# Performance work log

Hardware: AMD Instinct MI355X
Metric: run time of the kernel (lower is better)

Reference implementation:

```python
import jax, jax.numpy as jnp
import numpy as np

B, T, C, H = 4, 2048, 1024, 128

def setup_inputs() -> dict:
    key = jax.random.key(0)
    k1, k2, k3, k4 = jax.random.split(key, 4)
    x = jax.random.normal(k1, (B, T, C), dtype=jnp.float32)
    # nn.Linear(C, H, bias=False) weights, stored as [C, H] so y = x @ W
    scale = 1.0 / np.sqrt(C)
    Wq = jax.random.normal(k2, (C, H), dtype=jnp.float32) * scale
    Wk = jax.random.normal(k3, (C, H), dtype=jnp.float32) * scale
    Wv = jax.random.normal(k4, (C, H), dtype=jnp.float32) * scale
    mask = jnp.tril(jnp.ones((T, T), dtype=jnp.int32))  # causal mask
    return {"x": x, "Wq": Wq, "Wk": Wk, "Wv": Wv, "mask": mask}

def reference(x, Wq, Wk, Wv, mask):
    # x: [B,T,C]; projections to [B,T,H]
    q = jnp.einsum("btc,ch->bth", x, Wq)
    k = jnp.einsum("btc,ch->bth", x, Wk)
    v = jnp.einsum("btc,ch->bth", x, Wv)
    # NOTE: original scales by C**-0.5 (embedding dim), not head_size**-0.5
    inv_scale = x.shape[-1] ** (-0.5)
    scores = jnp.einsum("bth,bsh->bts", q, k) * inv_scale  # [B,T,T]
    scores = jnp.where(mask == 0, -jnp.inf, scores)
    weights = jax.nn.softmax(scores, axis=-1)
    # Dropout(0.1) is identity in eval mode
    return jnp.einsum("bts,bsh->bth", weights, v)  # [B,T,H]
```

## Files before the change

kernel.cpp:

```cpp
#include <hip/hip_runtime.h>
#include <hip/hip_bf16.h>
#include <cstdint>


typedef __bf16 bf16_t;
typedef __bf16 bf16x4 __attribute__((ext_vector_type(4)));
typedef __bf16 bf16x8 __attribute__((ext_vector_type(8)));
typedef float f32x4 __attribute__((ext_vector_type(4)));

#define MFMA16(a, b, c) __builtin_amdgcn_mfma_f32_16x16x32_bf16(a, b, c, 0, 0, 0)

constexpr int T = 2048;
constexpr int C = 1024;
constexpr int H = 128;
constexpr int BK = 64;

__device__ inline bf16x8 load8f(const float* __restrict__ p) {
    float4 a = *(const float4*)p;
    float4 b = *(const float4*)(p + 4);
    bf16x8 r;
    r[0] = (bf16_t)a.x; r[1] = (bf16_t)a.y; r[2] = (bf16_t)a.z; r[3] = (bf16_t)a.w;
    r[4] = (bf16_t)b.x; r[5] = (bf16_t)b.y; r[6] = (bf16_t)b.z; r[7] = (bf16_t)b.w;
    return r;
}

__device__ inline void gld16(const bf16_t* g, bf16_t* l) {
    __builtin_amdgcn_global_load_lds(
        (const __attribute__((address_space(1))) unsigned int*)g,
        (__attribute__((address_space(3))) unsigned int*)l, 16, 0, 0);
}

__global__ __launch_bounds__(256) void prep(const float* __restrict__ x,
                                            const float* __restrict__ Wq,
                                            const float* __restrict__ Wk,
                                            const float* __restrict__ Wv,
                                            bf16_t* __restrict__ xb,
                                            bf16_t* __restrict__ Wt) {
    const int t = threadIdx.x;
    if (blockIdx.x < 2048) {
        const int n8 = 4 * T * C / 8;
        int i = blockIdx.x * 256 + t;
        for (; i < n8; i += 2048 * 256)
            *(bf16x8*)(xb + (size_t)i * 8) = load8f(x + (size_t)i * 8);
    } else {
        __shared__ bf16_t tile[32][34];
        const int b2 = blockIdx.x - 2048;
        const int z = b2 >> 7, rem = b2 & 127;
        const int c0 = (rem & 31) * 32, h0 = (rem >> 5) * 32;
        const float* W = z == 0 ? Wq : (z == 1 ? Wk : Wv);
        const int tx = t & 31, ty = t >> 5;
#pragma unroll
        for (int i = 0; i < 4; i++)
            tile[ty + 8 * i][tx] = (bf16_t)W[(size_t)(c0 + ty + 8 * i) * H + h0 + tx];
        __syncthreads();
        bf16_t* Wtz = Wt + (size_t)z * H * C;
#pragma unroll
        for (int i = 0; i < 4; i++)
            Wtz[(size_t)(h0 + ty + 8 * i) * C + c0 + tx] = tile[tx][ty + 8 * i];
    }
}

__global__ __launch_bounds__(256) void proj_gemm(const bf16_t* __restrict__ xb,
                                                 const bf16_t* __restrict__ Wt,
                                                 bf16_t* __restrict__ qout,
                                                 bf16_t* __restrict__ kout,
                                                 bf16_t* __restrict__ vtout) {
    __shared__ __align__(16) bf16_t Ab[2][64 * BK];
    __shared__ __align__(16) bf16_t Bb[2][128 * BK];
    const int t = threadIdx.x;
    const int w = t >> 6, lane = t & 63;
    const int m16 = lane & 15, g = lane >> 4;
    const int wm = w & 1, wn = w >> 1;
    const int z = blockIdx.y;
    const int m0 = blockIdx.x * 64;
    const bf16_t* Bsrc = Wt + (size_t)z * H * C;

    auto stage = [&](int s, int k0) {
#pragma unroll
        for (int i = 0; i < 2; i++) {
            const int e = i * 256 + t;
            const int r = e >> 3, v = e & 7, c8 = v ^ (r & 7);
            gld16(xb + (size_t)(m0 + r) * C + k0 + c8 * 8,
                  &Ab[s][(i * 4 + w) * 512]);
        }
#pragma unroll
        for (int i = 0; i < 4; i++) {
            const int e = i * 256 + t;
            const int r = e >> 3, v = e & 7, c8 = v ^ (r & 7);
            gld16(Bsrc + (size_t)r * C + k0 + c8 * 8,
                  &Bb[s][(i * 4 + w) * 512]);
        }
    };

    f32x4 zero = {0.f, 0.f, 0.f, 0.f};
    f32x4 acc[2][4];
#pragma unroll
    for (int mf = 0; mf < 2; mf++)
#pragma unroll
        for (int nf = 0; nf < 4; nf++) acc[mf][nf] = zero;

    stage(0, 0);
    for (int c = 0; c < C / BK; c++) {
        __syncthreads();
        if (c + 1 < C / BK) stage((c + 1) & 1, (c + 1) * BK);
        const int s = c & 1;

        bf16x8 af[2][2], bfr[4][2];
#pragma unroll
        for (int mf = 0; mf < 2; mf++)
#pragma unroll
            for (int kf = 0; kf < 2; kf++) {
                const int r = wm * 32 + mf * 16 + m16;
                const int v = (kf * 4 + g) ^ (r & 7);
                af[mf][kf] = *(const bf16x8*)(&Ab[s][r * BK + v * 8]);
            }
#pragma unroll
        for (int nf = 0; nf < 4; nf++)
#pragma unroll
            for (int kf = 0; kf < 2; kf++) {
                const int r = wn * 64 + nf * 16 + m16;
                const int v = (kf * 4 + g) ^ (r & 7);
                bfr[nf][kf] = *(const bf16x8*)(&Bb[s][r * BK + v * 8]);
            }
#pragma unroll
        for (int kf = 0; kf < 2; kf++)
#pragma unroll
            for (int mf = 0; mf < 2; mf++)
#pragma unroll
                for (int nf = 0; nf < 4; nf++)
                    acc[mf][nf] = MFMA16(af[mf][kf], bfr[nf][kf], acc[mf][nf]);
    }

    const float sc = (z == 0) ? 0.03125f : 1.0f;
    if (z < 2) {
        bf16_t* out = (z == 0) ? qout : kout;
#pragma unroll
        for (int mf = 0; mf < 2; mf++)
#pragma unroll
            for (int nf = 0; nf < 4; nf++)
#pragma unroll
                for (int ri = 0; ri < 4; ri++) {
                    const int r = m0 + wm * 32 + mf * 16 + g * 4 + ri;
                    const int n = wn * 64 + nf * 16 + m16;
                    out[(size_t)r * H + n] = (bf16_t)(acc[mf][nf][ri] * sc);
                }
    } else {
#pragma unroll
        for (int mf = 0; mf < 2; mf++) {
            const int t0 = m0 + wm * 32 + mf * 16 + g * 4;
            const int bidx = t0 >> 11, tt = t0 & (T - 1);
#pragma unroll
            for (int nf = 0; nf < 4; nf++) {
                const int h = wn * 64 + nf * 16 + m16;
                bf16x4 vv;
#pragma unroll
                for (int ri = 0; ri < 4; ri++) vv[ri] = (bf16_t)acc[mf][nf][ri];
                *(bf16x4*)(vtout + ((size_t)bidx * H + h) * T + tt) = vv;
            }
        }
    }
}

__global__ __launch_bounds__(256) void attn(const bf16_t* __restrict__ q,
                                            const bf16_t* __restrict__ k,
                                            const bf16_t* __restrict__ vt,
                                            float* __restrict__ out) {
    __shared__ float accw[4][16][128];
    __shared__ __align__(16) bf16_t pbuf[4][16][40];
    __shared__ float mred[4][16], lred[4][16];
    const int w = threadIdx.x >> 6;
    const int lane = threadIdx.x & 63;
    const int m16 = lane & 15, g = lane >> 4;
    const int b = blockIdx.x & 3;
    const int kk = blockIdx.x >> 2;
    const int qt = (kk < 64) ? kk : 191 - kk;
    const int q0 = qt * 16;

    const bf16_t* qb = q + (size_t)b * T * H;
    const bf16_t* kb = k + (size_t)b * T * H;
    const bf16_t* vb = vt + (size_t)b * H * T;

    bf16x8 aq[4];
#pragma unroll
    for (int c = 0; c < 4; c++)
        aq[c] = *(const bf16x8*)(qb + (size_t)(q0 + m16) * H + c * 32 + g * 8);

    bf16x8 ones;
#pragma unroll
    for (int j = 0; j < 8; j++) ones[j] = (bf16_t)1.0f;

    f32x4 zero = {0.f, 0.f, 0.f, 0.f};
    f32x4 acc[9];
#pragma unroll
    for (int ht = 0; ht < 9; ht++) acc[ht] = zero;
    float mst[4];
#pragma unroll
    for (int ri = 0; ri < 4; ri++) mst[ri] = -1e30f;

    const int kv_end = q0 + 16;
    bf16x8 kc[8], kn[8], vc[8];
    int kv0 = w * 32;
    if (kv0 < kv_end) {
#pragma unroll
        for (int t = 0; t < 2; t++)
#pragma unroll
            for (int c = 0; c < 4; c++)
                kc[t * 4 + c] = *(const bf16x8*)(kb + (size_t)(kv0 + t * 16 + m16) * H + c * 32 + g * 8);
    }

    for (; kv0 < kv_end; kv0 += 128) {
        f32x4 s[2];
        s[0] = zero; s[1] = zero;
#pragma unroll
        for (int t = 0; t < 2; t++)
#pragma unroll
            for (int c = 0; c < 4; c++)
                s[t] = MFMA16(aq[c], kc[t * 4 + c], s[t]);

#pragma unroll
        for (int ht = 0; ht < 8; ht++)
            vc[ht] = *(const bf16x8*)(vb + (size_t)(ht * 16 + m16) * T + kv0 + g * 8);

        const int kvn = kv0 + 128;
        if (kvn < kv_end) {
#pragma unroll
            for (int t = 0; t < 2; t++)
#pragma unroll
                for (int c = 0; c < 4; c++)
                    kn[t * 4 + c] = *(const bf16x8*)(kb + (size_t)(kvn + t * 16 + m16) * H + c * 32 + g * 8);
        }

        float p0v[4], p1v[4];
#pragma unroll
        for (int ri = 0; ri < 4; ri++) {
            const int row = q0 + g * 4 + ri;
            float v0 = s[0][ri];
            float v1 = s[1][ri];
            if (kv0 + m16 > row) v0 = -1e30f;
            if (kv0 + 16 + m16 > row) v1 = -1e30f;
            float rm = fmaxf(v0, v1);
#pragma unroll
            for (int off = 1; off < 16; off <<= 1) rm = fmaxf(rm, __shfl_xor(rm, off));
            const float mnew = fmaxf(mst[ri], rm);
            const float alpha = __expf(mst[ri] - mnew);
            mst[ri] = mnew;
            p0v[ri] = __expf(v0 - mnew);
            p1v[ri] = __expf(v1 - mnew);
#pragma unroll
            for (int ht = 0; ht < 9; ht++) acc[ht][ri] *= alpha;
        }

#pragma unroll
        for (int ri = 0; ri < 4; ri++) {
            pbuf[w][g * 4 + ri][m16] = (bf16_t)p0v[ri];
            pbuf[w][g * 4 + ri][16 + m16] = (bf16_t)p1v[ri];
        }
        bf16x8 ap = *(const bf16x8*)(&pbuf[w][m16][g * 8]);

#pragma unroll
        for (int ht = 0; ht < 8; ht++)
            acc[ht] = MFMA16(ap, vc[ht], acc[ht]);
        acc[8] = MFMA16(ap, ones, acc[8]);

#pragma unroll
        for (int i = 0; i < 8; i++) kc[i] = kn[i];
    }

    if (m16 == 0) {
#pragma unroll
        for (int ri = 0; ri < 4; ri++) mred[w][g * 4 + ri] = mst[ri];
    }
    __syncthreads();
    float scale[4];
#pragma unroll
    for (int ri = 0; ri < 4; ri++) {
        const int row = g * 4 + ri;
        float mt = fmaxf(fmaxf(mred[0][row], mred[1][row]),
                         fmaxf(mred[2][row], mred[3][row]));
        scale[ri] = __expf(mst[ri] - mt);
    }
    if (m16 == 0) {
#pragma unroll
        for (int ri = 0; ri < 4; ri++) lred[w][g * 4 + ri] = acc[8][ri] * scale[ri];
    }
#pragma unroll
    for (int ht = 0; ht < 8; ht++)
#pragma unroll
        for (int ri = 0; ri < 4; ri++)
            accw[w][g * 4 + ri][ht * 16 + m16] = acc[ht][ri] * scale[ri];
    __syncthreads();

    float* ob = out + ((size_t)b * T + q0) * H;
    for (int e = threadIdx.x; e < 16 * 128; e += 256) {
        const int row = e >> 7, col = e & 127;
        float o = accw[0][row][col] + accw[1][row][col] +
                  accw[2][row][col] + accw[3][row][col];
        float l = lred[0][row] + lred[1][row] + lred[2][row] + lred[3][row];
        ob[(size_t)row * H + col] = o / l;
    }
}

extern "C" void kernel_launch(void* const* d_in, const int* in_sizes, int n_in,
                              void* d_out, int out_size, void* d_ws, size_t ws_size,
                              hipStream_t stream) {
    const float* x = (const float*)d_in[0];
    const float* Wq = (const float*)d_in[1];
    const float* Wk = (const float*)d_in[2];
    const float* Wv = (const float*)d_in[3];
    float* out = (float*)d_out;

    char* ws = (char*)d_ws;
    bf16_t* xb = (bf16_t*)ws;
    bf16_t* Wt = (bf16_t*)(ws + 16777216);
    char* p = ws + 16777216 + 786432;
    bf16_t* qb = (bf16_t*)(p);
    bf16_t* kb = (bf16_t*)(p + 2097152);
    bf16_t* vt = (bf16_t*)(p + 2 * 2097152);

    hipLaunchKernelGGL(prep, dim3(2048 + 384), dim3(256), 0, stream,
                       x, Wq, Wk, Wv, xb, Wt);
    hipLaunchKernelGGL(proj_gemm, dim3(128, 3), dim3(256), 0, stream,
                       xb, Wt, qb, kb, vt);
    hipLaunchKernelGGL(attn, dim3(512), dim3(256), 0, stream,
                       qb, kb, vt, out);
}
```

Baseline: 140.7 us.

## Process 32 query rows per attention block to reuse K/V loads

Measured after the change: 146.7 us. 1.04x slower.

```diff
diff --git a/kernel.cpp b/kernel.cpp
--- a/kernel.cpp
+++ b/kernel.cpp
@@ -80,15 +80,13 @@
         for (int i = 0; i < 2; i++) {
             const int e = i * 256 + t;
             const int r = e >> 3, v = e & 7, c8 = v ^ (r & 7);
-            gld16(xb + (size_t)(m0 + r) * C + k0 + c8 * 8,
-                  &Ab[s][(i * 4 + w) * 512]);
+            gld16(xb + (size_t)(m0 + r) * C + k0 + c8 * 8, &Ab[s][(i * 4 + w) * 512]);
         }
 #pragma unroll
         for (int i = 0; i < 4; i++) {
             const int e = i * 256 + t;
             const int r = e >> 3, v = e & 7, c8 = v ^ (r & 7);
-            gld16(Bsrc + (size_t)r * C + k0 + c8 * 8,
-                  &Bb[s][(i * 4 + w) * 512]);
+            gld16(Bsrc + (size_t)r * C + k0 + c8 * 8, &Bb[s][(i * 4 + w) * 512]);
         }
     };
 
@@ -161,43 +159,48 @@
     }
 }
 
-__global__ __launch_bounds__(256) void attn(const bf16_t* __restrict__ q,
-                                            const bf16_t* __restrict__ k,
-                                            const bf16_t* __restrict__ vt,
-                                            float* __restrict__ out) {
-    __shared__ float accw[4][16][128];
-    __shared__ __align__(16) bf16_t pbuf[4][16][40];
-    __shared__ float mred[4][16], lred[4][16];
+__global__ __launch_bounds__(256, 1) void attn(const bf16_t* __restrict__ q,
+                                               const bf16_t* __restrict__ k,
+                                               const bf16_t* __restrict__ vt,
+                                               float* __restrict__ out) {
+    __shared__ float accw[4][32][128];
+    __shared__ __align__(16) bf16_t pbuf[4][32][40];
+    __shared__ float mred[4][32], lred[4][32];
     const int w = threadIdx.x >> 6;
     const int lane = threadIdx.x & 63;
     const int m16 = lane & 15, g = lane >> 4;
     const int b = blockIdx.x & 3;
-    const int kk = blockIdx.x >> 2;
-    const int qt = (kk < 64) ? kk : 191 - kk;
-    const int q0 = qt * 16;
+    const int j = blockIdx.x >> 2;
+    const int q0 = j * 32;
 
     const bf16_t* qb = q + (size_t)b * T * H;
     const bf16_t* kb = k + (size_t)b * T * H;
     const bf16_t* vb = vt + (size_t)b * H * T;
 
-    bf16x8 aq[4];
-#pragma unroll
-    for (int c = 0; c < 4; c++)
-        aq[c] = *(const bf16x8*)(qb + (size_t)(q0 + m16) * H + c * 32 + g * 8);
+    bf16x8 aq[2][4];
+#pragma unroll
+    for (int mf = 0; mf < 2; mf++)
+#pragma unroll
+        for (int c = 0; c < 4; c++)
+            aq[mf][c] = *(const bf16x8*)(qb + (size_t)(q0 + mf * 16 + m16) * H + c * 32 + g * 8);
 
     bf16x8 ones;
 #pragma unroll
-    for (int j = 0; j < 8; j++) ones[j] = (bf16_t)1.0f;
+    for (int i = 0; i < 8; i++) ones[i] = (bf16_t)1.0f;
 
     f32x4 zero = {0.f, 0.f, 0.f, 0.f};
-    f32x4 acc[9];
-#pragma unroll
-    for (int ht = 0; ht < 9; ht++) acc[ht] = zero;
-    float mst[4];
-#pragma unroll
-    for (int ri = 0; ri < 4; ri++) mst[ri] = -1e30f;
-
-    const int kv_end = q0 + 16;
+    f32x4 acc[2][9];
+#pragma unroll
+    for (int mf = 0; mf < 2; mf++)
+#pragma unroll
+        for (int ht = 0; ht < 9; ht++) acc[mf][ht] = zero;
+    float mst[2][4];
+#pragma unroll
+    for (int mf = 0; mf < 2; mf++)
+#pragma unroll
+        for (int ri = 0; ri < 4; ri++) mst[mf][ri] = -1e30f;
+
+    const int kv_end = q0 + 32;
     bf16x8 kc[8], kn[8], vc[8];
     int kv0 = w * 32;
     if (kv0 < kv_end) {
@@ -209,18 +212,21 @@
     }
 
     for (; kv0 < kv_end; kv0 += 128) {
-        f32x4 s[2];
-        s[0] = zero; s[1] = zero;
+        f32x4 s[2][2];
+#pragma unroll
+        for (int mf = 0; mf < 2; mf++) { s[mf][0] = zero; s[mf][1] = zero; }
 #pragma unroll
         for (int t = 0; t < 2; t++)
 #pragma unroll
-            for (int c = 0; c < 4; c++)
-                s[t] = MFMA16(aq[c], kc[t * 4 + c], s[t]);
+            for (int c = 0; c < 4; c++) {
+#pragma unroll
+                for (int mf = 0; mf < 2; mf++)
+                    s[mf][t] = MFMA16(aq[mf][c], kc[t * 4 + c], s[mf][t]);
+            }
 
 #pragma unroll
         for (int ht = 0; ht < 8; ht++)
             vc[ht] = *(const bf16x8*)(vb + (size_t)(ht * 16 + m16) * T + kv0 + g * 8);
-
         const int kvn = kv0 + 128;
         if (kvn < kv_end) {
 #pragma unroll
@@ -230,68 +236,80 @@
                     kn[t * 4 + c] = *(const bf16x8*)(kb + (size_t)(kvn + t * 16 + m16) * H + c * 32 + g * 8);
         }
 
-        float p0v[4], p1v[4];
+#pragma unroll
+        for (int mf = 0; mf < 2; mf++) {
+            float p0v[4], p1v[4];
+#pragma unroll
+            for (int ri = 0; ri < 4; ri++) {
+                const int row = q0 + mf * 16 + g * 4 + ri;
+                float v0 = s[mf][0][ri];
+                float v1 = s[mf][1][ri];
+                if (kv0 + m16 > row) v0 = -1e30f;
+                if (kv0 + 16 + m16 > row) v1 = -1e30f;
+                float rm = fmaxf(v0, v1);
+#pragma unroll
+                for (int off = 1; off < 16; off <<= 1) rm = fmaxf(rm, __shfl_xor(rm, off));
+                const float mnew = fmaxf(mst[mf][ri], rm);
+                const float alpha = __expf(mst[mf][ri] - mnew);
+                mst[mf][ri] = mnew;
+                p0v[ri] = __expf(v0 - mnew);
+                p1v[ri] = __expf(v1 - mnew);
+#pragma unroll
+                for (int ht = 0; ht < 9; ht++) acc[mf][ht][ri] *= alpha;
+            }
+#pragma unroll
+            for (int ri = 0; ri < 4; ri++) {
+                pbuf[w][mf * 16 + g * 4 + ri][m16] = (bf16_t)p0v[ri];
+                pbuf[w][mf * 16 + g * 4 + ri][16 + m16] = (bf16_t)p1v[ri];
+            }
+        }
+
+#pragma unroll
+        for (int mf = 0; mf < 2; mf++) {
+            bf16x8 ap = *(const bf16x8*)(&pbuf[w][mf * 16 + m16][g * 8]);
+#pragma unroll
+            for (int ht = 0; ht < 8; ht++)
+                acc[mf][ht] = MFMA16(ap, vc[ht], acc[mf][ht]);
+            acc[mf][8] = MFMA16(ap, ones, acc[mf][8]);
+        }
+
+#pragma unroll
+        for (int i = 0; i < 8; i++) kc[i] = kn[i];
+    }
+
+    if (m16 == 0) {
+#pragma unroll
+        for (int mf = 0; mf < 2; mf++)
+#pragma unroll
+            for (int ri = 0; ri < 4; ri++)
+                mred[w][mf * 16 + g * 4 + ri] = mst[mf][ri];
+    }
+    __syncthreads();
+#pragma unroll
+    for (int mf = 0; mf < 2; mf++) {
+        float scale[4];
 #pragma unroll
         for (int ri = 0; ri < 4; ri++) {
-            const int row = q0 + g * 4 + ri;
-            float v0 = s[0][ri];
-            float v1 = s[1][ri];
-            if (kv0 + m16 > row) v0 = -1e30f;
-            if (kv0 + 16 + m16 > row) v1 = -1e30f;
-            float rm = fmaxf(v0, v1);
-#pragma unroll
-            for (int off = 1; off < 16; off <<= 1) rm = fmaxf(rm, __shfl_xor(rm, off));
-            const float mnew = fmaxf(mst[ri], rm);
-            const float alpha = __expf(mst[ri] - mnew);
-            mst[ri] = mnew;
-            p0v[ri] = __expf(v0 - mnew);
-            p1v[ri] = __expf(v1 - mnew);
-#pragma unroll
-            for (int ht = 0; ht < 9; ht++) acc[ht][ri] *= alpha;
-        }
-
-#pragma unroll
-        for (int ri = 0; ri < 4; ri++) {
-            pbuf[w][g * 4 + ri][m16] = (bf16_t)p0v[ri];
-            pbuf[w][g * 4 + ri][16 + m16] = (bf16_t)p1v[ri];
-        }
-        bf16x8 ap = *(const bf16x8*)(&pbuf[w][m16][g * 8]);
-
+            const int row = mf * 16 + g * 4 + ri;
+            float mt = fmaxf(fmaxf(mred[0][row], mred[1][row]),
+                             fmaxf(mred[2][row], mred[3][row]));
+            scale[ri] = __expf(mst[mf][ri] - mt);
+        }
+        if (m16 == 0) {
+#pragma unroll
+            for (int ri = 0; ri < 4; ri++)
+                lred[w][mf * 16 + g * 4 + ri] = acc[mf][8][ri] * scale[ri];
+        }
 #pragma unroll
         for (int ht = 0; ht < 8; ht++)
-            acc[ht] = MFMA16(ap, vc[ht], acc[ht]);
-        acc[8] = MFMA16(ap, ones, acc[8]);
-
-#pragma unroll
-        for (int i = 0; i < 8; i++) kc[i] = kn[i];
-    }
-
-    if (m16 == 0) {
-#pragma unroll
-        for (int ri = 0; ri < 4; ri++) mred[w][g * 4 + ri] = mst[ri];
+#pragma unroll
+            for (int ri = 0; ri < 4; ri++)
+                accw[w][mf * 16 + g * 4 + ri][ht * 16 + m16] = acc[mf][ht][ri] * scale[ri];
     }
     __syncthreads();
-    float scale[4];
-#pragma unroll
-    for (int ri = 0; ri < 4; ri++) {
-        const int row = g * 4 + ri;
-        float mt = fmaxf(fmaxf(mred[0][row], mred[1][row]),
-                         fmaxf(mred[2][row], mred[3][row]));
-        scale[ri] = __expf(mst[ri] - mt);
-    }
-    if (m16 == 0) {
-#pragma unroll
-        for (int ri = 0; ri < 4; ri++) lred[w][g * 4 + ri] = acc[8][ri] * scale[ri];
-    }
-#pragma unroll
-    for (int ht = 0; ht < 8; ht++)
-#pragma unroll
-        for (int ri = 0; ri < 4; ri++)
-            accw[w][g * 4 + ri][ht * 16 + m16] = acc[ht][ri] * scale[ri];
-    __syncthreads();
 
     float* ob = out + ((size_t)b * T + q0) * H;
-    for (int e = threadIdx.x; e < 16 * 128; e += 256) {
+    for (int e = threadIdx.x; e < 32 * 128; e += 256) {
         const int row = e >> 7, col = e & 127;
         float o = accw[0][row][col] + accw[1][row][col] +
                   accw[2][row][col] + accw[3][row][col];
@@ -321,6 +339,6 @@
                        x, Wq, Wk, Wv, xb, Wt);
     hipLaunchKernelGGL(proj_gemm, dim3(128, 3), dim3(256), 0, stream,
                        xb, Wt, qb, kb, vt);
-    hipLaunchKernelGGL(attn, dim3(512), dim3(256), 0, stream,
+    hipLaunchKernelGGL(attn, dim3(256), dim3(256), 0, stream,
                        qb, kb, vt, out);
 }
```

## Fuse prep, projection GEMM and attention into one persistent kernel with grid barriers

Applied to the files above, without the earlier changes.

New measurement: 322.6 us. 129% more time.

```diff
diff --git a/kernel.cpp b/kernel.cpp
--- a/kernel.cpp
+++ b/kernel.cpp
@@ -15,288 +15,299 @@
 constexpr int H = 128;
 constexpr int BK = 64;
 
-__device__ inline bf16x8 load8f(const float* __restrict__ p) {
-    float4 a = *(const float4*)p;
-    float4 b = *(const float4*)(p + 4);
-    bf16x8 r;
-    r[0] = (bf16_t)a.x; r[1] = (bf16_t)a.y; r[2] = (bf16_t)a.z; r[3] = (bf16_t)a.w;
-    r[4] = (bf16_t)b.x; r[5] = (bf16_t)b.y; r[6] = (bf16_t)b.z; r[7] = (bf16_t)b.w;
-    return r;
-}
-
-__device__ inline void gld16(const bf16_t* g, bf16_t* l) {
+__device__ inline void gld16(const void* g, void* l) {
     __builtin_amdgcn_global_load_lds(
         (const __attribute__((address_space(1))) unsigned int*)g,
         (__attribute__((address_space(3))) unsigned int*)l, 16, 0, 0);
 }
 
-__global__ __launch_bounds__(256) void prep(const float* __restrict__ x,
-                                            const float* __restrict__ Wq,
-                                            const float* __restrict__ Wk,
-                                            const float* __restrict__ Wv,
-                                            bf16_t* __restrict__ xb,
-                                            bf16_t* __restrict__ Wt) {
-    const int t = threadIdx.x;
-    if (blockIdx.x < 2048) {
-        const int n8 = 4 * T * C / 8;
-        int i = blockIdx.x * 256 + t;
-        for (; i < n8; i += 2048 * 256)
-            *(bf16x8*)(xb + (size_t)i * 8) = load8f(x + (size_t)i * 8);
-    } else {
-        __shared__ bf16_t tile[32][34];
-        const int b2 = blockIdx.x - 2048;
-        const int z = b2 >> 7, rem = b2 & 127;
+__device__ inline void gbar(int* cnt, int target) {
+    __syncthreads();
+    if (threadIdx.x == 0) {
+        __threadfence();
+        __hip_atomic_fetch_add(cnt, 1, __ATOMIC_ACQ_REL, __HIP_MEMORY_SCOPE_AGENT);
+        while (__hip_atomic_load(cnt, __ATOMIC_ACQUIRE, __HIP_MEMORY_SCOPE_AGENT) < target)
+            __builtin_amdgcn_s_sleep(8);
+        __threadfence();
+    }
+    __syncthreads();
+}
+
+union SMem {
+    struct { bf16_t tile[32][34]; } tr;
+    struct { float Ab[2][64 * BK]; bf16_t Bb[2][128 * BK]; } pj;
+    struct {
+        float accw[4][16][128];
+        bf16_t pbuf[4][16][40];
+        float mred[4][16], lred[4][16];
+    } at;
+};
+
+__global__ __launch_bounds__(256, 2) void fused(const float* __restrict__ x,
+                                                const float* __restrict__ Wq,
+                                                const float* __restrict__ Wk,
+                                                const float* __restrict__ Wv,
+                                                bf16_t* __restrict__ Wt,
+                                                bf16_t* __restrict__ qb_,
+                                                bf16_t* __restrict__ kb_,
+                                                bf16_t* __restrict__ vt_,
+                                                float* __restrict__ out,
+                                                int* __restrict__ flag) {
+    __shared__ __align__(16) SMem sm;
+    const int tid = threadIdx.x;
+    const int blk = blockIdx.x;
+
+    if (blk < 384) {
+        const int z = blk >> 7, rem = blk & 127;
         const int c0 = (rem & 31) * 32, h0 = (rem >> 5) * 32;
         const float* W = z == 0 ? Wq : (z == 1 ? Wk : Wv);
-        const int tx = t & 31, ty = t >> 5;
+        const int tx = tid & 31, ty = tid >> 5;
 #pragma unroll
         for (int i = 0; i < 4; i++)
-            tile[ty + 8 * i][tx] = (bf16_t)W[(size_t)(c0 + ty + 8 * i) * H + h0 + tx];
+            sm.tr.tile[ty + 8 * i][tx] = (bf16_t)W[(size_t)(c0 + ty + 8 * i) * H + h0 + tx];
         __syncthreads();
         bf16_t* Wtz = Wt + (size_t)z * H * C;
 #pragma unroll
         for (int i = 0; i < 4; i++)
-            Wtz[(size_t)(h0 + ty + 8 * i) * C + c0 + tx] = tile[tx][ty + 8 * i];
+            Wtz[(size_t)(h0 + ty + 8 * i) * C + c0 + tx] = sm.tr.tile[tx][ty + 8 * i];
     }
-}
-
-__global__ __launch_bounds__(256) void proj_gemm(const bf16_t* __restrict__ xb,
-                                                 const bf16_t* __restrict__ Wt,
-                                                 bf16_t* __restrict__ qout,
-                                                 bf16_t* __restrict__ kout,
-                                                 bf16_t* __restrict__ vtout) {
-    __shared__ __align__(16) bf16_t Ab[2][64 * BK];
-    __shared__ __align__(16) bf16_t Bb[2][128 * BK];
-    const int t = threadIdx.x;
-    const int w = t >> 6, lane = t & 63;
-    const int m16 = lane & 15, g = lane >> 4;
-    const int wm = w & 1, wn = w >> 1;
-    const int z = blockIdx.y;
-    const int m0 = blockIdx.x * 64;
-    const bf16_t* Bsrc = Wt + (size_t)z * H * C;
-
-    auto stage = [&](int s, int k0) {
-#pragma unroll
-        for (int i = 0; i < 2; i++) {
-            const int e = i * 256 + t;
-            const int r = e >> 3, v = e & 7, c8 = v ^ (r & 7);
-            gld16(xb + (size_t)(m0 + r) * C + k0 + c8 * 8,
-                  &Ab[s][(i * 4 + w) * 512]);
-        }
-#pragma unroll
-        for (int i = 0; i < 4; i++) {
-            const int e = i * 256 + t;
-            const int r = e >> 3, v = e & 7, c8 = v ^ (r & 7);
-            gld16(Bsrc + (size_t)r * C + k0 + c8 * 8,
-                  &Bb[s][(i * 4 + w) * 512]);
-        }
-    };
-
-    f32x4 zero = {0.f, 0.f, 0.f, 0.f};
-    f32x4 acc[2][4];
-#pragma unroll
-    for (int mf = 0; mf < 2; mf++)
-#pragma unroll
-        for (int nf = 0; nf < 4; nf++) acc[mf][nf] = zero;
-
-    stage(0, 0);
-    for (int c = 0; c < C / BK; c++) {
+    gbar(flag, 512);
+
+    if (blk < 384) {
+        const int w = tid >> 6, lane = tid & 63;
+        const int m16 = lane & 15, g = lane >> 4;
+        const int wm = w & 1, wn = w >> 1;
+        const int z = blk >> 7;
+        const int m0 = (blk & 127) * 64;
+        const bf16_t* Bsrc = Wt + (size_t)z * H * C;
+
+        auto stage = [&](int s, int k0) {
+#pragma unroll
+            for (int i = 0; i < 4; i++) {
+                const int e = i * 256 + tid;
+                const int r = e >> 4, v = e & 15, c4 = v ^ (r & 15);
+                gld16(x + (size_t)(m0 + r) * C + k0 + c4 * 4,
+                      &sm.pj.Ab[s][(i * 4 + w) * 256]);
+            }
+#pragma unroll
+            for (int i = 0; i < 4; i++) {
+                const int e = i * 256 + tid;
+                const int r = e >> 3, v = e & 7, c8 = v ^ (r & 7);
+                gld16(Bsrc + (size_t)r * C + k0 + c8 * 8,
+                      &sm.pj.Bb[s][(i * 4 + w) * 512]);
+            }
+        };
+
+        f32x4 zero = {0.f, 0.f, 0.f, 0.f};
+        f32x4 acc[2][4];
+#pragma unroll
+        for (int mf = 0; mf < 2; mf++)
+#pragma unroll
+            for (int nf = 0; nf < 4; nf++) acc[mf][nf] = zero;
+
+        stage(0, 0);
+        for (int c = 0; c < C / BK; c++) {
+            __syncthreads();
+            if (c + 1 < C / BK) stage((c + 1) & 1, (c + 1) * BK);
+            const int s = c & 1;
+
+            bf16x8 af[2][2], bfr[4][2];
+#pragma unroll
+            for (int mf = 0; mf < 2; mf++)
+#pragma unroll
+                for (int kf = 0; kf < 2; kf++) {
+                    const int r = wm * 32 + mf * 16 + m16;
+                    const int c4 = kf * 8 + g * 2;
+                    const int va = c4 ^ (r & 15), vb = (c4 + 1) ^ (r & 15);
+                    float4 fa = *(const float4*)(&sm.pj.Ab[s][r * BK + va * 4]);
+                    float4 fb = *(const float4*)(&sm.pj.Ab[s][r * BK + vb * 4]);
+                    bf16x8 t;
+                    t[0] = (bf16_t)fa.x; t[1] = (bf16_t)fa.y;
+                    t[2] = (bf16_t)fa.z; t[3] = (bf16_t)fa.w;
+                    t[4] = (bf16_t)fb.x; t[5] = (bf16_t)fb.y;
+                    t[6] = (bf16_t)fb.z; t[7] = (bf16_t)fb.w;
+                    af[mf][kf] = t;
+                }
+#pragma unroll
+            for (int nf = 0; nf < 4; nf++)
+#pragma unroll
+                for (int kf = 0; kf < 2; kf++) {
+                    const int r = wn * 64 + nf * 16 + m16;
+                    const int v = (kf * 4 + g) ^ (r & 7);
+                    bfr[nf][kf] = *(const bf16x8*)(&sm.pj.Bb[s][r * BK + v * 8]);
+                }
+#pragma unroll
+            for (int kf = 0; kf < 2; kf++)
+#pragma unroll
+                for (int mf = 0; mf < 2; mf++)
+#pragma unroll
+                    for (int nf = 0; nf < 4; nf++)
+                        acc[mf][nf] = MFMA16(af[mf][kf], bfr[nf][kf], acc[mf][nf]);
+        }
+
+        const float sc = (z == 0) ? 0.03125f : 1.0f;
+        if (z < 2) {
+            bf16_t* o = (z == 0) ? qb_ : kb_;
+#pragma unroll
+            for (int mf = 0; mf < 2; mf++)
+#pragma unroll
+                for (int nf = 0; nf < 4; nf++)
+#pragma unroll
+                    for (int ri = 0; ri < 4; ri++) {
+                        const int r = m0 + wm * 32 + mf * 16 + g * 4 + ri;
+                        const int n = wn * 64 + nf * 16 + m16;
+                        o[(size_t)r * H + n] = (bf16_t)(acc[mf][nf][ri] * sc);
+                    }
+        } else {
+#pragma unroll
+            for (int mf = 0; mf < 2; mf++) {
+                const int t0 = m0 + wm * 32 + mf * 16 + g * 4;
+                const int bidx = t0 >> 11, tt = t0 & (T - 1);
+#pragma unroll
+                for (int nf = 0; nf < 4; nf++) {
+                    const int h = wn * 64 + nf * 16 + m16;
+                    bf16x4 vv;
+#pragma unroll
+                    for (int ri = 0; ri < 4; ri++) vv[ri] = (bf16_t)acc[mf][nf][ri];
+                    *(bf16x4*)(vt_ + ((size_t)bidx * H + h) * T + tt) = vv;
+                }
+            }
+        }
+    }
+    gbar(flag, 1024);
+
+    {
+        const int w = tid >> 6;
+        const int lane = tid & 63;
+        const int m16 = lane & 15, g = lane >> 4;
+        const int b = blk & 3;
+        const int kk = blk >> 2;
+        const int qt = (kk < 64) ? kk : 191 - kk;
+        const int q0 = qt * 16;
+
+        const bf16_t* qb = qb_ + (size_t)b * T * H;
+        const bf16_t* kb = kb_ + (size_t)b * T * H;
+        const bf16_t* vb = vt_ + (size_t)b * H * T;
+
+        bf16x8 aq[4];
+#pragma unroll
+        for (int c = 0; c < 4; c++)
+            aq[c] = *(const bf16x8*)(qb + (size_t)(q0 + m16) * H + c * 32 + g * 8);
+
+        bf16x8 ones;
+#pragma unroll
+        for (int i = 0; i < 8; i++) ones[i] = (bf16_t)1.0f;
+
+        f32x4 zero = {0.f, 0.f, 0.f, 0.f};
+        f32x4 acc[9];
+#pragma unroll
+        for (int ht = 0; ht < 9; ht++) acc[ht] = zero;
+        float mst[4];
+#pragma unroll
+        for (int ri = 0; ri < 4; ri++) mst[ri] = -1e30f;
+
+        const int kv_end = q0 + 16;
+        bf16x8 kc[8], kn[8], vc[8];
+        int kv0 = w * 32;
+        if (kv0 < kv_end) {
+#pragma unroll
+            for (int t = 0; t < 2; t++)
+#pragma unroll
+                for (int c = 0; c < 4; c++)
+                    kc[t * 4 + c] = *(const bf16x8*)(kb + (size_t)(kv0 + t * 16 + m16) * H + c * 32 + g * 8);
+        }
+
+        for (; kv0 < kv_end; kv0 += 128) {
+            f32x4 s[2];
+            s[0] = zero; s[1] = zero;
+#pragma unroll
+            for (int t = 0; t < 2; t++)
+#pragma unroll
+                for (int c = 0; c < 4; c++)
+                    s[t] = MFMA16(aq[c], kc[t * 4 + c], s[t]);
+
+#pragma unroll
+            for (int ht = 0; ht < 8; ht++)
+                vc[ht] = *(const bf16x8*)(vb + (size_t)(ht * 16 + m16) * T + kv0 + g * 8);
+
+            const int kvn = kv0 + 128;
+            if (kvn < kv_end) {
+#pragma unroll
+                for (int t = 0; t < 2; t++)
+#pragma unroll
+                    for (int c = 0; c < 4; c++)
+                        kn[t * 4 + c] = *(const bf16x8*)(kb + (size_t)(kvn + t * 16 + m16) * H + c * 32 + g * 8);
+            }
+
+            float p0v[4], p1v[4];
+#pragma unroll
+            for (int ri = 0; ri < 4; ri++) {
+                const int row = q0 + g * 4 + ri;
+                float v0 = s[0][ri];
+                float v1 = s[1][ri];
+                if (kv0 + m16 > row) v0 = -1e30f;
+                if (kv0 + 16 + m16 > row) v1 = -1e30f;
+                float rm = fmaxf(v0, v1);
+#pragma unroll
+                for (int off = 1; off < 16; off <<= 1) rm = fmaxf(rm, __shfl_xor(rm, off));
+                const float mnew = fmaxf(mst[ri], rm);
+                const float alpha = __expf(mst[ri] - mnew);
+                mst[ri] = mnew;
+                p0v[ri] = __expf(v0 - mnew);
+                p1v[ri] = __expf(v1 - mnew);
+#pragma unroll
+                for (int ht = 0; ht < 9; ht++) acc[ht][ri] *= alpha;
+            }
+
+#pragma unroll
+            for (int ri = 0; ri < 4; ri++) {
+                sm.at.pbuf[w][g * 4 + ri][m16] = (bf16_t)p0v[ri];
+                sm.at.pbuf[w][g * 4 + ri][16 + m16] = (bf16_t)p1v[ri];
+            }
+            bf16x8 ap = *(const bf16x8*)(&sm.at.pbuf[w][m16][g * 8]);
+
+#pragma unroll
+            for (int ht = 0; ht < 8; ht++)
+                acc[ht] = MFMA16(ap, vc[ht], acc[ht]);
+            acc[8] = MFMA16(ap, ones, acc[8]);
+
+#pragma unroll
+            for (int i = 0; i < 8; i++) kc[i] = kn[i];
+        }
+
+        if (m16 == 0) {
+#pragma unroll
+            for (int ri = 0; ri < 4; ri++) sm.at.mred[w][g * 4 + ri] = mst[ri];
+        }
         __syncthreads();
-        if (c + 1 < C / BK) stage((c + 1) & 1, (c + 1) * BK);
-        const int s = c & 1;
-
-        bf16x8 af[2][2], bfr[4][2];
-#pragma unroll
-        for (int mf = 0; mf < 2; mf++)
-#pragma unroll
-            for (int kf = 0; kf < 2; kf++) {
-                const int r = wm * 32 + mf * 16 + m16;
-                const int v = (kf * 4 + g) ^ (r & 7);
-                af[mf][kf] = *(const bf16x8*)(&Ab[s][r * BK + v * 8]);
-            }
-#pragma unroll
-        for (int nf = 0; nf < 4; nf++)
-#pragma unroll
-            for (int kf = 0; kf < 2; kf++) {
-                const int r = wn * 64 + nf * 16 + m16;
-                const int v = (kf * 4 + g) ^ (r & 7);
-                bfr[nf][kf] = *(const bf16x8*)(&Bb[s][r * BK + v * 8]);
-            }
-#pragma unroll
-        for (int kf = 0; kf < 2; kf++)
-#pragma unroll
-            for (int mf = 0; mf < 2; mf++)
-#pragma unroll
-                for (int nf = 0; nf < 4; nf++)
-                    acc[mf][nf] = MFMA16(af[mf][kf], bfr[nf][kf], acc[mf][nf]);
-    }
-
-    const float sc = (z == 0) ? 0.03125f : 1.0f;
-    if (z < 2) {
-        bf16_t* out = (z == 0) ? qout : kout;
-#pragma unroll
-        for (int mf = 0; mf < 2; mf++)
-#pragma unroll
-            for (int nf = 0; nf < 4; nf++)
-#pragma unroll
-                for (int ri = 0; ri < 4; ri++) {
-                    const int r = m0 + wm * 32 + mf * 16 + g * 4 + ri;
-                    const int n = wn * 64 + nf * 16 + m16;
-                    out[(size_t)r * H + n] = (bf16_t)(acc[mf][nf][ri] * sc);
-                }
-    } else {
-#pragma unroll
-        for (int mf = 0; mf < 2; mf++) {
-            const int t0 = m0 + wm * 32 + mf * 16 + g * 4;
-            const int bidx = t0 >> 11, tt = t0 & (T - 1);
-#pragma unroll
-            for (int nf = 0; nf < 4; nf++) {
-                const int h = wn * 64 + nf * 16 + m16;
-                bf16x4 vv;
-#pragma unroll
-                for (int ri = 0; ri < 4; ri++) vv[ri] = (bf16_t)acc[mf][nf][ri];
-                *(bf16x4*)(vtout + ((size_t)bidx * H + h) * T + tt) = vv;
-            }
-        }
-    }
-}
-
-__global__ __launch_bounds__(256) void attn(const bf16_t* __restrict__ q,
-                                            const bf16_t* __restrict__ k,
-                                            const bf16_t* __restrict__ vt,
-                                            float* __restrict__ out) {
-    __shared__ float accw[4][16][128];
-    __shared__ __align__(16) bf16_t pbuf[4][16][40];
-    __shared__ float mred[4][16], lred[4][16];
-    const int w = threadIdx.x >> 6;
-    const int lane = threadIdx.x & 63;
-    const int m16 = lane & 15, g = lane >> 4;
-    const int b = blockIdx.x & 3;
-    const int kk = blockIdx.x >> 2;
-    const int qt = (kk < 64) ? kk : 191 - kk;
-    const int q0 = qt * 16;
-
-    const bf16_t* qb = q + (size_t)b * T * H;
-    const bf16_t* kb = k + (size_t)b * T * H;
-    const bf16_t* vb = vt + (size_t)b * H * T;
-
-    bf16x8 aq[4];
-#pragma unroll
-    for (int c = 0; c < 4; c++)
-        aq[c] = *(const bf16x8*)(qb + (size_t)(q0 + m16) * H + c * 32 + g * 8);
-
-    bf16x8 ones;
-#pragma unroll
-    for (int j = 0; j < 8; j++) ones[j] = (bf16_t)1.0f;
-
-    f32x4 zero = {0.f, 0.f, 0.f, 0.f};
-    f32x4 acc[9];
-#pragma unroll
-    for (int ht = 0; ht < 9; ht++) acc[ht] = zero;
-    float mst[4];
-#pragma unroll
-    for (int ri = 0; ri < 4; ri++) mst[ri] = -1e30f;
-
-    const int kv_end = q0 + 16;
-    bf16x8 kc[8], kn[8], vc[8];
-    int kv0 = w * 32;
-    if (kv0 < kv_end) {
-#pragma unroll
-        for (int t = 0; t < 2; t++)
-#pragma unroll
-            for (int c = 0; c < 4; c++)
-                kc[t * 4 + c] = *(const bf16x8*)(kb + (size_t)(kv0 + t * 16 + m16) * H + c * 32 + g * 8);
-    }
-
-    for (; kv0 < kv_end; kv0 += 128) {
-        f32x4 s[2];
-        s[0] = zero; s[1] = zero;
-#pragma unroll
-        for (int t = 0; t < 2; t++)
-#pragma unroll
-            for (int c = 0; c < 4; c++)
-                s[t] = MFMA16(aq[c], kc[t * 4 + c], s[t]);
-
+        float scale[4];
+#pragma unroll
+        for (int ri = 0; ri < 4; ri++) {
+            const int row = g * 4 + ri;
+            float mt = fmaxf(fmaxf(sm.at.mred[0][row], sm.at.mred[1][row]),
+                             fmaxf(sm.at.mred[2][row], sm.at.mred[3][row]));
+            scale[ri] = __expf(mst[ri] - mt);
+        }
+        if (m16 == 0) {
+#pragma unroll
+            for (int ri = 0; ri < 4; ri++) sm.at.lred[w][g * 4 + ri] = acc[8][ri] * scale[ri];
+        }
 #pragma unroll
         for (int ht = 0; ht < 8; ht++)
-            vc[ht] = *(const bf16x8*)(vb + (size_t)(ht * 16 + m16) * T + kv0 + g * 8);
-
-        const int kvn = kv0 + 128;
-        if (kvn < kv_end) {
-#pragma unroll
-            for (int t = 0; t < 2; t++)
-#pragma unroll
-                for (int c = 0; c < 4; c++)
-                    kn[t * 4 + c] = *(const bf16x8*)(kb + (size_t)(kvn + t * 16 + m16) * H + c * 32 + g * 8);
-        }
-
-        float p0v[4], p1v[4];
-#pragma unroll
-        for (int ri = 0; ri < 4; ri++) {
-            const int row = q0 + g * 4 + ri;
-            float v0 = s[0][ri];
-            float v1 = s[1][ri];
-            if (kv0 + m16 > row) v0 = -1e30f;
-            if (kv0 + 16 + m16 > row) v1 = -1e30f;
-            float rm = fmaxf(v0, v1);
-#pragma unroll
-            for (int off = 1; off < 16; off <<= 1) rm = fmaxf(rm, __shfl_xor(rm, off));
-            const float mnew = fmaxf(mst[ri], rm);
-            const float alpha = __expf(mst[ri] - mnew);
-            mst[ri] = mnew;
-            p0v[ri] = __expf(v0 - mnew);
-            p1v[ri] = __expf(v1 - mnew);
-#pragma unroll
-            for (int ht = 0; ht < 9; ht++) acc[ht][ri] *= alpha;
-        }
-
-#pragma unroll
-        for (int ri = 0; ri < 4; ri++) {
-            pbuf[w][g * 4 + ri][m16] = (bf16_t)p0v[ri];
-            pbuf[w][g * 4 + ri][16 + m16] = (bf16_t)p1v[ri];
-        }
-        bf16x8 ap = *(const bf16x8*)(&pbuf[w][m16][g * 8]);
-
-#pragma unroll
-        for (int ht = 0; ht < 8; ht++)
-            acc[ht] = MFMA16(ap, vc[ht], acc[ht]);
-        acc[8] = MFMA16(ap, ones, acc[8]);
-
-#pragma unroll
-        for (int i = 0; i < 8; i++) kc[i] = kn[i];
-    }
-
-    if (m16 == 0) {
-#pragma unroll
-        for (int ri = 0; ri < 4; ri++) mred[w][g * 4 + ri] = mst[ri];
-    }
-    __syncthreads();
-    float scale[4];
-#pragma unroll
-    for (int ri = 0; ri < 4; ri++) {
-        const int row = g * 4 + ri;
-        float mt = fmaxf(fmaxf(mred[0][row], mred[1][row]),
-                         fmaxf(mred[2][row], mred[3][row]));
-        scale[ri] = __expf(mst[ri] - mt);
-    }
-    if (m16 == 0) {
-#pragma unroll
-        for (int ri = 0; ri < 4; ri++) lred[w][g * 4 + ri] = acc[8][ri] * scale[ri];
-    }
-#pragma unroll
-    for (int ht = 0; ht < 8; ht++)
-#pragma unroll
-        for (int ri = 0; ri < 4; ri++)
-            accw[w][g * 4 + ri][ht * 16 + m16] = acc[ht][ri] * scale[ri];
-    __syncthreads();
-
-    float* ob = out + ((size_t)b * T + q0) * H;
-    for (int e = threadIdx.x; e < 16 * 128; e += 256) {
-        const int row = e >> 7, col = e & 127;
-        float o = accw[0][row][col] + accw[1][row][col] +
-                  accw[2][row][col] + accw[3][row][col];
-        float l = lred[0][row] + lred[1][row] + lred[2][row] + lred[3][row];
-        ob[(size_t)row * H + col] = o / l;
+#pragma unroll
+            for (int ri = 0; ri < 4; ri++)
+                sm.at.accw[w][g * 4 + ri][ht * 16 + m16] = acc[ht][ri] * scale[ri];
+        __syncthreads();
+
+        float* ob = out + ((size_t)b * T + q0) * H;
+        for (int e = tid; e < 16 * 128; e += 256) {
+            const int row = e >> 7, col = e & 127;
+            float o = sm.at.accw[0][row][col] + sm.at.accw[1][row][col] +
+                      sm.at.accw[2][row][col] + sm.at.accw[3][row][col];
+            float l = sm.at.lred[0][row] + sm.at.lred[1][row] +
+                      sm.at.lred[2][row] + sm.at.lred[3][row];
+            ob[(size_t)row * H + col] = o / l;
+        }
     }
 }
 
@@ -310,17 +321,14 @@
     float* out = (float*)d_out;
 
     char* ws = (char*)d_ws;
-    bf16_t* xb = (bf16_t*)ws;
-    bf16_t* Wt = (bf16_t*)(ws + 16777216);
-    char* p = ws + 16777216 + 786432;
+    bf16_t* Wt = (bf16_t*)ws;
+    char* p = ws + 786432;
     bf16_t* qb = (bf16_t*)(p);
     bf16_t* kb = (bf16_t*)(p + 2097152);
     bf16_t* vt = (bf16_t*)(p + 2 * 2097152);
-
-    hipLaunchKernelGGL(prep, dim3(2048 + 384), dim3(256), 0, stream,
-                       x, Wq, Wk, Wv, xb, Wt);
-    hipLaunchKernelGGL(proj_gemm, dim3(128, 3), dim3(256), 0, stream,
-                       xb, Wt, qb, kb, vt);
-    hipLaunchKernelGGL(attn, dim3(512), dim3(256), 0, stream,
-                       qb, kb, vt, out);
+    int* flag = (int*)(p + 3 * 2097152);
+
+    hipMemsetAsync(flag, 0, 4, stream);
+    hipLaunchKernelGGL(fused, dim3(512), dim3(256), 0, stream,
+                       x, Wq, Wk, Wv, Wt, qb, kb, vt, out, flag);
 }
```

## Fuse x bf16 conversion into projection GEMM and widen attention to 8 waves

Applied to the files above, without the earlier changes.

After: 167.0 us. +18.7%, slower.

```diff
diff --git a/kernel.cpp b/kernel.cpp
--- a/kernel.cpp
+++ b/kernel.cpp
@@ -15,60 +15,41 @@
 constexpr int H = 128;
 constexpr int BK = 64;
 
-__device__ inline bf16x8 load8f(const float* __restrict__ p) {
-    float4 a = *(const float4*)p;
-    float4 b = *(const float4*)(p + 4);
-    bf16x8 r;
-    r[0] = (bf16_t)a.x; r[1] = (bf16_t)a.y; r[2] = (bf16_t)a.z; r[3] = (bf16_t)a.w;
-    r[4] = (bf16_t)b.x; r[5] = (bf16_t)b.y; r[6] = (bf16_t)b.z; r[7] = (bf16_t)b.w;
-    return r;
-}
-
-__device__ inline void gld16(const bf16_t* g, bf16_t* l) {
+__device__ inline void gld16(const void* g, void* l) {
     __builtin_amdgcn_global_load_lds(
         (const __attribute__((address_space(1))) unsigned int*)g,
         (__attribute__((address_space(3))) unsigned int*)l, 16, 0, 0);
 }
 
-__global__ __launch_bounds__(256) void prep(const float* __restrict__ x,
-                                            const float* __restrict__ Wq,
-                                            const float* __restrict__ Wk,
-                                            const float* __restrict__ Wv,
-                                            bf16_t* __restrict__ xb,
-                                            bf16_t* __restrict__ Wt) {
-    const int t = threadIdx.x;
-    if (blockIdx.x < 2048) {
-        const int n8 = 4 * T * C / 8;
-        int i = blockIdx.x * 256 + t;
-        for (; i < n8; i += 2048 * 256)
-            *(bf16x8*)(xb + (size_t)i * 8) = load8f(x + (size_t)i * 8);
-    } else {
-        __shared__ bf16_t tile[32][34];
-        const int b2 = blockIdx.x - 2048;
-        const int z = b2 >> 7, rem = b2 & 127;
-        const int c0 = (rem & 31) * 32, h0 = (rem >> 5) * 32;
-        const float* W = z == 0 ? Wq : (z == 1 ? Wk : Wv);
-        const int tx = t & 31, ty = t >> 5;
-#pragma unroll
-        for (int i = 0; i < 4; i++)
-            tile[ty + 8 * i][tx] = (bf16_t)W[(size_t)(c0 + ty + 8 * i) * H + h0 + tx];
-        __syncthreads();
-        bf16_t* Wtz = Wt + (size_t)z * H * C;
-#pragma unroll
-        for (int i = 0; i < 4; i++)
-            Wtz[(size_t)(h0 + ty + 8 * i) * C + c0 + tx] = tile[tx][ty + 8 * i];
-    }
-}
-
-__global__ __launch_bounds__(256) void proj_gemm(const bf16_t* __restrict__ xb,
+__global__ __launch_bounds__(256) void transpose_w(const float* __restrict__ Wq,
+                                                   const float* __restrict__ Wk,
+                                                   const float* __restrict__ Wv,
+                                                   bf16_t* __restrict__ Wt) {
+    __shared__ bf16_t tile[32][34];
+    const int tid = threadIdx.x, blk = blockIdx.x;
+    const int z = blk >> 7, rem = blk & 127;
+    const int c0 = (rem & 31) * 32, h0 = (rem >> 5) * 32;
+    const float* W = z == 0 ? Wq : (z == 1 ? Wk : Wv);
+    const int tx = tid & 31, ty = tid >> 5;
+#pragma unroll
+    for (int i = 0; i < 4; i++)
+        tile[ty + 8 * i][tx] = (bf16_t)W[(size_t)(c0 + ty + 8 * i) * H + h0 + tx];
+    __syncthreads();
+    bf16_t* Wtz = Wt + (size_t)z * H * C;
+#pragma unroll
+    for (int i = 0; i < 4; i++)
+        Wtz[(size_t)(h0 + ty + 8 * i) * C + c0 + tx] = tile[tx][ty + 8 * i];
+}
+
+__global__ __launch_bounds__(256) void proj_gemm(const float* __restrict__ x,
                                                  const bf16_t* __restrict__ Wt,
                                                  bf16_t* __restrict__ qout,
                                                  bf16_t* __restrict__ kout,
                                                  bf16_t* __restrict__ vtout) {
-    __shared__ __align__(16) bf16_t Ab[2][64 * BK];
+    __shared__ __align__(16) float Ab[2][64 * BK];
     __shared__ __align__(16) bf16_t Bb[2][128 * BK];
-    const int t = threadIdx.x;
-    const int w = t >> 6, lane = t & 63;
+    const int tid = threadIdx.x;
+    const int w = tid >> 6, lane = tid & 63;
     const int m16 = lane & 15, g = lane >> 4;
     const int wm = w & 1, wn = w >> 1;
     const int z = blockIdx.y;
@@ -77,18 +58,16 @@
 
     auto stage = [&](int s, int k0) {
 #pragma unroll
-        for (int i = 0; i < 2; i++) {
-            const int e = i * 256 + t;
+        for (int i = 0; i < 4; i++) {
+            const int e = i * 256 + tid;
+            const int r = e >> 4, v = e & 15, c4 = v ^ (r & 15);
+            gld16(x + (size_t)(m0 + r) * C + k0 + c4 * 4, &Ab[s][(i * 4 + w) * 256]);
+        }
+#pragma unroll
+        for (int i = 0; i < 4; i++) {
+            const int e = i * 256 + tid;
             const int r = e >> 3, v = e & 7, c8 = v ^ (r & 7);
-            gld16(xb + (size_t)(m0 + r) * C + k0 + c8 * 8,
-                  &Ab[s][(i * 4 + w) * 512]);
-        }
-#pragma unroll
-        for (int i = 0; i < 4; i++) {
-            const int e = i * 256 + t;
-            const int r = e >> 3, v = e & 7, c8 = v ^ (r & 7);
-            gld16(Bsrc + (size_t)r * C + k0 + c8 * 8,
-                  &Bb[s][(i * 4 + w) * 512]);
+            gld16(Bsrc + (size_t)r * C + k0 + c8 * 8, &Bb[s][(i * 4 + w) * 512]);
         }
     };
 
@@ -111,8 +90,16 @@
 #pragma unroll
             for (int kf = 0; kf < 2; kf++) {
                 const int r = wm * 32 + mf * 16 + m16;
-                const int v = (kf * 4 + g) ^ (r & 7);
-                af[mf][kf] = *(const bf16x8*)(&Ab[s][r * BK + v * 8]);
+                const int c4 = kf * 8 + g * 2;
+                const int va = c4 ^ (r & 15), vb = (c4 + 1) ^ (r & 15);
+                float4 fa = *(const float4*)(&Ab[s][r * BK + va * 4]);
+                float4 fb = *(const float4*)(&Ab[s][r * BK + vb * 4]);
+                bf16x8 t;
+                t[0] = (bf16_t)fa.x; t[1] = (bf16_t)fa.y;
+                t[2] = (bf16_t)fa.z; t[3] = (bf16_t)fa.w;
+                t[4] = (bf16_t)fb.x; t[5] = (bf16_t)fb.y;
+                t[6] = (bf16_t)fb.z; t[7] = (bf16_t)fb.w;
+                af[mf][kf] = t;
             }
 #pragma unroll
         for (int nf = 0; nf < 4; nf++)
@@ -133,7 +120,7 @@
 
     const float sc = (z == 0) ? 0.03125f : 1.0f;
     if (z < 2) {
-        bf16_t* out = (z == 0) ? qout : kout;
+        bf16_t* o = (z == 0) ? qout : kout;
 #pragma unroll
         for (int mf = 0; mf < 2; mf++)
 #pragma unroll
@@ -142,7 +129,7 @@
                 for (int ri = 0; ri < 4; ri++) {
                     const int r = m0 + wm * 32 + mf * 16 + g * 4 + ri;
                     const int n = wn * 64 + nf * 16 + m16;
-                    out[(size_t)r * H + n] = (bf16_t)(acc[mf][nf][ri] * sc);
+                    o[(size_t)r * H + n] = (bf16_t)(acc[mf][nf][ri] * sc);
                 }
     } else {
 #pragma unroll
@@ -161,15 +148,16 @@
     }
 }
 
-__global__ __launch_bounds__(256) void attn(const bf16_t* __restrict__ q,
-                                            const bf16_t* __restrict__ k,
-                                            const bf16_t* __restrict__ vt,
-                                            float* __restrict__ out) {
-    __shared__ float accw[4][16][128];
-    __shared__ __align__(16) bf16_t pbuf[4][16][40];
-    __shared__ float mred[4][16], lred[4][16];
-    const int w = threadIdx.x >> 6;
-    const int lane = threadIdx.x & 63;
+__global__ __launch_bounds__(512, 4) void attn(const bf16_t* __restrict__ q,
+                                               const bf16_t* __restrict__ k,
+                                               const bf16_t* __restrict__ vt,
+                                               float* __restrict__ out) {
+    __shared__ float buf[4][16][128];
+    __shared__ __align__(16) bf16_t pbuf[8][16][40];
+    __shared__ float mred[8][16], lred[8][16];
+    const int tid = threadIdx.x;
+    const int w = tid >> 6;
+    const int lane = tid & 63;
     const int m16 = lane & 15, g = lane >> 4;
     const int b = blockIdx.x & 3;
     const int kk = blockIdx.x >> 2;
@@ -187,7 +175,7 @@
 
     bf16x8 ones;
 #pragma unroll
-    for (int j = 0; j < 8; j++) ones[j] = (bf16_t)1.0f;
+    for (int i = 0; i < 8; i++) ones[i] = (bf16_t)1.0f;
 
     f32x4 zero = {0.f, 0.f, 0.f, 0.f};
     f32x4 acc[9];
@@ -208,7 +196,7 @@
                 kc[t * 4 + c] = *(const bf16x8*)(kb + (size_t)(kv0 + t * 16 + m16) * H + c * 32 + g * 8);
     }
 
-    for (; kv0 < kv_end; kv0 += 128) {
+    for (; kv0 < kv_end; kv0 += 256) {
         f32x4 s[2];
         s[0] = zero; s[1] = zero;
 #pragma unroll
@@ -221,7 +209,7 @@
         for (int ht = 0; ht < 8; ht++)
             vc[ht] = *(const bf16x8*)(vb + (size_t)(ht * 16 + m16) * T + kv0 + g * 8);
 
-        const int kvn = kv0 + 128;
+        const int kvn = kv0 + 256;
         if (kvn < kv_end) {
 #pragma unroll
             for (int t = 0; t < 2; t++)
@@ -275,8 +263,9 @@
 #pragma unroll
     for (int ri = 0; ri < 4; ri++) {
         const int row = g * 4 + ri;
-        float mt = fmaxf(fmaxf(mred[0][row], mred[1][row]),
-                         fmaxf(mred[2][row], mred[3][row]));
+        float mt = mred[0][row];
+#pragma unroll
+        for (int j = 1; j < 8; j++) mt = fmaxf(mt, mred[j][row]);
         scale[ri] = __expf(mst[ri] - mt);
     }
     if (m16 == 0) {
@@ -286,17 +275,62 @@
 #pragma unroll
     for (int ht = 0; ht < 8; ht++)
 #pragma unroll
-        for (int ri = 0; ri < 4; ri++)
-            accw[w][g * 4 + ri][ht * 16 + m16] = acc[ht][ri] * scale[ri];
-    __syncthreads();
-
-    float* ob = out + ((size_t)b * T + q0) * H;
-    for (int e = threadIdx.x; e < 16 * 128; e += 256) {
-        const int row = e >> 7, col = e & 127;
-        float o = accw[0][row][col] + accw[1][row][col] +
-                  accw[2][row][col] + accw[3][row][col];
-        float l = lred[0][row] + lred[1][row] + lred[2][row] + lred[3][row];
-        ob[(size_t)row * H + col] = o / l;
+        for (int ri = 0; ri < 4; ri++) acc[ht][ri] *= scale[ri];
+
+    if (w >= 4) {
+#pragma unroll
+        for (int ht = 0; ht < 8; ht++)
+#pragma unroll
+            for (int ri = 0; ri < 4; ri++)
+                buf[w - 4][g * 4 + ri][ht * 16 + m16] = acc[ht][ri];
+    }
+    __syncthreads();
+    if (w < 4) {
+#pragma unroll
+        for (int ht = 0; ht < 8; ht++)
+#pragma unroll
+            for (int ri = 0; ri < 4; ri++)
+                acc[ht][ri] += buf[w][g * 4 + ri][ht * 16 + m16];
+    }
+    __syncthreads();
+    if (w == 2 || w == 3) {
+#pragma unroll
+        for (int ht = 0; ht < 8; ht++)
+#pragma unroll
+            for (int ri = 0; ri < 4; ri++)
+                buf[w - 2][g * 4 + ri][ht * 16 + m16] = acc[ht][ri];
+    }
+    __syncthreads();
+    if (w < 2) {
+#pragma unroll
+        for (int ht = 0; ht < 8; ht++)
+#pragma unroll
+            for (int ri = 0; ri < 4; ri++)
+                acc[ht][ri] += buf[w][g * 4 + ri][ht * 16 + m16];
+    }
+    __syncthreads();
+    if (w == 1) {
+#pragma unroll
+        for (int ht = 0; ht < 8; ht++)
+#pragma unroll
+            for (int ri = 0; ri < 4; ri++)
+                buf[1][g * 4 + ri][ht * 16 + m16] = acc[ht][ri];
+    }
+    __syncthreads();
+    if (w == 0) {
+        float* ob = out + ((size_t)b * T + q0) * H;
+#pragma unroll
+        for (int ri = 0; ri < 4; ri++) {
+            const int row = g * 4 + ri;
+            float lt = lred[0][row];
+#pragma unroll
+            for (int j = 1; j < 8; j++) lt += lred[j][row];
+            const float inv = 1.f / lt;
+#pragma unroll
+            for (int ht = 0; ht < 8; ht++)
+                ob[(size_t)row * H + ht * 16 + m16] =
+                    (acc[ht][ri] + buf[1][row][ht * 16 + m16]) * inv;
+        }
     }
 }
 
@@ -310,17 +344,16 @@
     float* out = (float*)d_out;
 
     char* ws = (char*)d_ws;
-    bf16_t* xb = (bf16_t*)ws;
-    bf16_t* Wt = (bf16_t*)(ws + 16777216);
-    char* p = ws + 16777216 + 786432;
+    bf16_t* Wt = (bf16_t*)ws;
+    char* p = ws + 786432;
     bf16_t* qb = (bf16_t*)(p);
     bf16_t* kb = (bf16_t*)(p + 2097152);
     bf16_t* vt = (bf16_t*)(p + 2 * 2097152);
 
-    hipLaunchKernelGGL(prep, dim3(2048 + 384), dim3(256), 0, stream,
-                       x, Wq, Wk, Wv, xb, Wt);
+    hipLaunchKernelGGL(transpose_w, dim3(384), dim3(256), 0, stream,
+                       Wq, Wk, Wv, Wt);
     hipLaunchKernelGGL(proj_gemm, dim3(128, 3), dim3(256), 0, stream,
-                       xb, Wt, qb, kb, vt);
-    hipLaunchKernelGGL(attn, dim3(512), dim3(256), 0, stream,
+                       x, Wt, qb, kb, vt);
+    hipLaunchKernelGGL(attn, dim3(512), dim3(512), 0, stream,
                        qb, kb, vt, out);
 }
```
